# Kernel optimization log

Measured on AMD Instinct MI355X. Metric: run time of the kernel, lower is better.

## Reference

```python
import jax, jax.numpy as jnp
import numpy as np

LEAKAGE = 0.9
RADIUS = 0.1
AVG_DEGREE = 6


def setup_inputs() -> dict:
    key = jax.random.key(0)
    k1, k2, k3, k4, k5 = jax.random.split(key, 5)
    B, T, I, N, O = 16, 2048, 32, 2048, 32
    input_sequence = jax.random.normal(k1, (B, T, I), dtype=jnp.float32)
    # sparse reservoir matrix, uniform(-1,1) with density avg_degree/N, scaled to spectral radius
    A = jax.random.uniform(k2, (N, N), minval=-1.0, maxval=1.0, dtype=jnp.float32)
    mask = jax.random.uniform(k3, (N, N)) < (AVG_DEGREE / N)
    A = jnp.where(mask, A, 0.0)
    # approximate spectral normalization (power-iteration-free surrogate scale)
    A = A * (RADIUS / jnp.max(jnp.abs(jnp.linalg.eigvals(A))).astype(jnp.float32))
    Win = (RADIUS) * (2.0 * jax.random.uniform(k4, (N, I), dtype=jnp.float32) - 1.0)
    Wout_w = jax.random.normal(k5, (O, N), dtype=jnp.float32) / np.sqrt(N)
    return {"input_sequence": input_sequence, "Win": Win, "A": A, "Wout_w": Wout_w, "washout_len": 64}


def reference(input_sequence, Win, A, Wout_w, washout_len):
    # input projection for all timesteps at once (noise_std = 0.0)
    inp = jnp.einsum('bti,ni->btn', input_sequence, Win)  # [B, T, N]
    B = input_sequence.shape[0]
    N = A.shape[0]
    h0 = jnp.zeros((B, N), dtype=input_sequence.dtype)
    At = A.T

    def step(h, u_t):
        # h: [B, N], u_t: [B, N]
        h_new = (1.0 - LEAKAGE) * h + LEAKAGE * jnp.tanh(h @ At + u_t)
        return h_new, h_new

    _, hs = jax.lax.scan(step, h0, jnp.swapaxes(inp, 0, 1))  # hs: [T, B, N]
    hs = jnp.swapaxes(hs, 0, 1)  # [B, T, N]
    h_list = hs[:, washout_len - 1:]  # keep steps i >= washout_len - 1
    return jnp.einsum('btn,on->bto', h_list, Wout_w)
```

## Files before the change

kernel.cpp:

```cpp
#include <hip/hip_runtime.h>
#include <stdint.h>

#define BB 16
#define TT 2048
#define NI 32
#define NN 2048
#define NO 32
#define WASH 64
#define TO (TT - WASH + 1)
#define W 24
#define CH 16
#define UST 18
#define HBST 2056

typedef short bfvec __attribute__((ext_vector_type(8)));
typedef float f4_t  __attribute__((ext_vector_type(4)));

__device__ inline unsigned short f2bf(float f) {
  unsigned int u = __builtin_bit_cast(unsigned int, f);
  unsigned int r = u + 0x7fffu + ((u >> 16) & 1u);
  return (unsigned short)(r >> 16);
}
__device__ inline float bf2f(unsigned short s) {
  unsigned int u = ((unsigned int)s) << 16;
  return __builtin_bit_cast(float, u);
}
__device__ inline float tanh_fast(float x) {
  x = fminf(15.f, fmaxf(-15.f, x));
  float e = __expf(x + x);
  return (e - 1.0f) / (e + 1.0f);
}

__global__ void build_ell(const float* __restrict__ A, uint32_t* __restrict__ ell,
                          uint32_t* __restrict__ deg) {
  int gw = (int)((blockIdx.x * blockDim.x + threadIdx.x) >> 6);
  int lane = (int)(threadIdx.x & 63);
  if (gw >= NN) return;
  const float* row = A + (size_t)gw * NN;
  int base = 0;
  for (int c = 0; c < NN; c += 64) {
    float v = row[c + lane];
    bool nz = (v != 0.0f);
    unsigned long long mask = __ballot(nz);
    int pre = __popcll(mask & ((1ull << lane) - 1ull));
    if (nz) {
      int idx = base + pre;
      if (idx < W) {
        uint32_t packed = (((uint32_t)f2bf(v)) << 16) | (uint32_t)((c + lane) * 4);
        ell[(size_t)gw * W + idx] = packed;
      }
    }
    base += __popcll(mask);
  }
  int d = base < W ? base : W;
  if (lane == 0) deg[gw] = (uint32_t)d;
  for (int k = d + lane; k < W; k += 64) ell[(size_t)gw * W + k] = 0u;
}

__global__ void sortperm(const uint32_t* __restrict__ deg, uint32_t* __restrict__ perm) {
  __shared__ unsigned int hist[32];
  __shared__ unsigned int off[32];
  int tid = (int)threadIdx.x;
  if (tid < 32) hist[tid] = 0;
  __syncthreads();
  for (int r = tid; r < NN; r += 1024) {
    unsigned int d = deg[r]; if (d > 31u) d = 31u;
    atomicAdd(&hist[d], 1u);
  }
  __syncthreads();
  if (tid == 0) {
    unsigned int s = 0;
    for (int i = 0; i < 32; ++i) { off[i] = s; s += hist[i]; }
  }
  __syncthreads();
  for (int r = tid; r < NN; r += 1024) {
    unsigned int d = deg[r]; if (d > 31u) d = 31u;
    unsigned int p = atomicAdd(&off[d], 1u);
    perm[p] = (uint32_t)r;
  }
}

__global__ void build_frags(const float* __restrict__ Win, const float* __restrict__ Wout,
                            uint32_t* __restrict__ winf, uint32_t* __restrict__ woutf) {
  int f = (int)(blockIdx.x * blockDim.x + threadIdx.x);
  if (f < 32768) {
    int reg = f & 3, lane = (f >> 2) & 63, ntg = f >> 8;
    int n = (ntg << 4) + (lane & 15);
    int k = ((lane >> 4) << 3) + reg * 2;
    uint32_t lo = f2bf(Win[(size_t)n * NI + k]);
    uint32_t hi = f2bf(Win[(size_t)n * NI + k + 1]);
    winf[f] = lo | (hi << 16);
  } else {
    int g = f - 32768;
    int reg = g & 3, lane = (g >> 2) & 63, kt = (g >> 8) & 63, ot = g >> 14;
    int o = (ot << 4) + (lane & 15);
    int n = (kt << 5) + ((lane >> 4) << 3) + reg * 2;
    uint32_t lo = f2bf(Wout[(size_t)o * NN + n]);
    uint32_t hi = f2bf(Wout[(size_t)o * NN + n + 1]);
    woutf[g] = lo | (hi << 16);
  }
}

__global__ __launch_bounds__(1024, 1) void rec_kernel(
    const float* __restrict__ x, const uint32_t* __restrict__ ell,
    const uint32_t* __restrict__ deg, const uint32_t* __restrict__ perm,
    const uint32_t* __restrict__ winf, const uint32_t* __restrict__ woutf,
    float* __restrict__ out) {
  extern __shared__ char smem[];
  float* h_a = (float*)smem;
  float* h_b = (float*)(smem + 8192);
  unsigned short* u_lds = (unsigned short*)(smem + 16384);
  float* oscratch = (float*)(smem + 16384);
  unsigned short* hb = (unsigned short*)(smem + 16384 + 73728);

  const int tid = (int)threadIdx.x;
  const int b = (int)blockIdx.x;
  const int lane = tid & 63;
  const int wv = tid >> 6;

  const int r0 = (int)perm[tid];
  const int r1 = (int)perm[2047 - tid];
  int d0 = (int)deg[r0], d1 = (int)deg[r1];
  int m0 = d0, m1 = d1;
  #pragma unroll
  for (int off = 32; off; off >>= 1) {
    m0 = max(m0, __shfl_xor(m0, off));
    m1 = max(m1, __shfl_xor(m1, off));
  }
  m0 = __builtin_amdgcn_readfirstlane(m0);
  m1 = __builtin_amdgcn_readfirstlane(m1);

  uint32_t e0[W], e1[W];
  {
    const uint4* p0 = (const uint4*)(ell + (size_t)r0 * W);
    const uint4* p1 = (const uint4*)(ell + (size_t)r1 * W);
    #pragma unroll
    for (int q = 0; q < W / 4; ++q) {
      uint4 a = p0[q]; uint4 c = p1[q];
      e0[q*4+0]=a.x; e0[q*4+1]=a.y; e0[q*4+2]=a.z; e0[q*4+3]=a.w;
      e1[q*4+0]=c.x; e1[q*4+1]=c.y; e1[q*4+2]=c.z; e1[q*4+3]=c.w;
    }
  }

  h_a[tid] = 0.0f; h_a[tid + 1024] = 0.0f;
  float h0 = 0.0f, h1 = 0.0f;

  const int la15 = lane & 15;
  const int lg = lane >> 4;

  auto step = [&](int tt, const float* hcur, float* hnxt) {
    float y0 = bf2f(u_lds[(size_t)r0 * UST + tt]);
    float y1 = bf2f(u_lds[(size_t)r1 * UST + tt]);
    #pragma unroll
    for (int k = 0; k < W; ++k) {
      if (k >= m0) break;
      uint32_t e = e0[k];
      float v = __builtin_bit_cast(float, e & 0xffff0000u);
      float hv = *(const float*)((const char*)hcur + (e & 0xffffu));
      y0 = __builtin_fmaf(v, hv, y0);
    }
    #pragma unroll
    for (int k = 0; k < W; ++k) {
      if (k >= m1) break;
      uint32_t e = e1[k];
      float v = __builtin_bit_cast(float, e & 0xffff0000u);
      float hv = *(const float*)((const char*)hcur + (e & 0xffffu));
      y1 = __builtin_fmaf(v, hv, y1);
    }
    float hn0 = 0.1f * h0 + 0.9f * tanh_fast(y0);
    float hn1 = 0.1f * h1 + 0.9f * tanh_fast(y1);
    hnxt[r0] = hn0; hnxt[r1] = hn1;
    hb[(size_t)tt * HBST + r0] = f2bf(hn0);
    hb[(size_t)tt * HBST + r1] = f2bf(hn1);
    h0 = hn0; h1 = hn1;
    __syncthreads();
  };

  for (int c = 0; c < TT / CH; ++c) {
    const int t0 = c * CH;

    {
      const float* xp = x + ((size_t)b * TT + (t0 + la15)) * NI + (lg << 3);
      float4 x0 = *(const float4*)xp;
      float4 x1 = *(const float4*)(xp + 4);
      union { unsigned short u16[8]; bfvec v; } af;
      af.u16[0]=f2bf(x0.x); af.u16[1]=f2bf(x0.y); af.u16[2]=f2bf(x0.z); af.u16[3]=f2bf(x0.w);
      af.u16[4]=f2bf(x1.x); af.u16[5]=f2bf(x1.y); af.u16[6]=f2bf(x1.z); af.u16[7]=f2bf(x1.w);
      #pragma unroll
      for (int nt = 0; nt < 8; ++nt) {
        int ntg = (wv << 3) + nt;
        union { uint4 q; bfvec v; } bw;
        bw.q = *(const uint4*)(winf + (((size_t)ntg * 64 + lane) << 2));
        f4_t acc = {0.f, 0.f, 0.f, 0.f};
        acc = __builtin_amdgcn_mfma_f32_16x16x32_bf16(af.v, bw.v, acc, 0, 0, 0);
        int n = (ntg << 4) + la15;
        int tl = lg << 2;
        uint32_t lo = (uint32_t)f2bf(acc[0]) | ((uint32_t)f2bf(acc[1]) << 16);
        uint32_t hi = (uint32_t)f2bf(acc[2]) | ((uint32_t)f2bf(acc[3]) << 16);
        uint32_t* up = (uint32_t*)(u_lds + (size_t)n * UST + tl);
        up[0] = lo; up[1] = hi;
      }
    }
    __syncthreads();

    #pragma unroll 1
    for (int tt = 0; tt < CH; tt += 2) {
      step(tt, h_a, h_b);
      step(tt + 1, h_b, h_a);
    }

    {
      f4_t oa0 = {0.f,0.f,0.f,0.f}, oa1 = {0.f,0.f,0.f,0.f};
      #pragma unroll
      for (int k4 = 0; k4 < 4; ++k4) {
        int kt = (wv << 2) + k4;
        union { uint4 q; bfvec v; } ha, w0, w1;
        ha.q = *(const uint4*)(hb + (size_t)la15 * HBST + (kt << 5) + (lg << 3));
        w0.q = *(const uint4*)(woutf + (((size_t)(kt) * 64 + lane) << 2));
        w1.q = *(const uint4*)(woutf + (((size_t)(64 + kt) * 64 + lane) << 2));
        oa0 = __builtin_amdgcn_mfma_f32_16x16x32_bf16(ha.v, w0.v, oa0, 0, 0, 0);
        oa1 = __builtin_amdgcn_mfma_f32_16x16x32_bf16(ha.v, w1.v, oa1, 0, 0, 0);
      }
      float* os = oscratch + (wv << 9);
      int tb = lg << 2;
      #pragma unroll
      for (int r = 0; r < 4; ++r) os[(tb + r) * 32 + la15] = oa0[r];
      #pragma unroll
      for (int r = 0; r < 4; ++r) os[(tb + r) * 32 + 16 + la15] = oa1[r];
    }
    __syncthreads();
    if (tid < 512) {
      float s = 0.0f;
      #pragma unroll
      for (int w2 = 0; w2 < 16; ++w2) s += oscratch[(w2 << 9) + tid];
      int tg = t0 + (tid >> 5);
      if (tg >= WASH - 1)
        out[((size_t)b * TO + (tg - (WASH - 1))) * NO + (tid & 31)] = s;
    }
    __syncthreads();
  }
}

extern "C" void kernel_launch(void* const* d_in, const int* in_sizes, int n_in,
                              void* d_out, int out_size, void* d_ws, size_t ws_size,
                              hipStream_t stream) {
  (void)in_sizes; (void)n_in; (void)out_size; (void)ws_size;
  const float* x    = (const float*)d_in[0];
  const float* Win  = (const float*)d_in[1];
  const float* A    = (const float*)d_in[2];
  const float* Wout = (const float*)d_in[3];
  float* out = (float*)d_out;

  char* ws = (char*)d_ws;
  uint32_t* ell   = (uint32_t*)(ws);
  uint32_t* deg   = (uint32_t*)(ws + 196608);
  uint32_t* perm  = (uint32_t*)(ws + 204800);
  uint32_t* winf  = (uint32_t*)(ws + 212992);
  uint32_t* woutf = (uint32_t*)(ws + 344064);

  hipFuncSetAttribute((const void*)rec_kernel,
                      hipFuncAttributeMaxDynamicSharedMemorySize, 160 * 1024);

  hipLaunchKernelGGL(build_ell, dim3(512), dim3(256), 0, stream, A, ell, deg);
  hipLaunchKernelGGL(sortperm, dim3(1), dim3(1024), 0, stream, deg, perm);
  hipLaunchKernelGGL(build_frags, dim3(256), dim3(256), 0, stream, Win, Wout, winf, woutf);
  hipLaunchKernelGGL(rec_kernel, dim3(16), dim3(1024), 155904, stream,
                     x, ell, deg, perm, winf, woutf, out);
}
```

Baseline: 3.063 ms.

## Renumber reservoir rows by degree and schedule ELL gathers to avoid LDS bank conflicts

```diff
diff --git a/kernel.cpp b/kernel.cpp
--- a/kernel.cpp
+++ b/kernel.cpp
@@ -57,53 +57,107 @@
   for (int k = d + lane; k < W; k += 64) ell[(size_t)gw * W + k] = 0u;
 }
 
-__global__ void sortperm(const uint32_t* __restrict__ deg, uint32_t* __restrict__ perm) {
-  __shared__ unsigned int hist[32];
-  __shared__ unsigned int off[32];
+__global__ void sortperm(const uint32_t* __restrict__ deg, uint32_t* __restrict__ perm,
+                         uint32_t* __restrict__ invp) {
+  __shared__ int dg[NN];
   int tid = (int)threadIdx.x;
-  if (tid < 32) hist[tid] = 0;
+  dg[tid] = (int)deg[tid];
+  dg[tid + 1024] = (int)deg[tid + 1024];
   __syncthreads();
   for (int r = tid; r < NN; r += 1024) {
-    unsigned int d = deg[r]; if (d > 31u) d = 31u;
-    atomicAdd(&hist[d], 1u);
+    int d = dg[r];
+    int rank = 0;
+    for (int j = 0; j < NN; ++j) {
+      int dj = dg[j];
+      rank += (dj < d) || (dj == d && j < r);
+    }
+    perm[rank] = (uint32_t)r;
+    invp[r] = (uint32_t)rank;
+  }
+}
+
+__global__ void schedule_ell(const uint32_t* __restrict__ ell_in, const uint32_t* __restrict__ deg,
+                             const uint32_t* __restrict__ perm, const uint32_t* __restrict__ invp,
+                             uint32_t* __restrict__ ell_out, uint32_t* __restrict__ slen) {
+  __shared__ uint32_t ent[64][W];
+  __shared__ uint32_t outp[64][W];
+  __shared__ int nent[64];
+  __shared__ uint32_t used[64];
+  __shared__ int Ssh;
+  int blk = (int)blockIdx.x;
+  int t = (int)threadIdx.x;
+  int rs = blk * 64 + t;
+  int ro = (int)perm[rs];
+  int d = (int)deg[ro]; if (d > W) d = W;
+  nent[t] = d; used[t] = 0u;
+  for (int k = 0; k < d; ++k) {
+    uint32_t e = ell_in[(size_t)ro * W + k];
+    uint32_t col = (e & 0xffffu) >> 2;
+    uint32_t cs = invp[col];
+    ent[t][k] = (e & 0xffff0000u) | (cs << 2);
   }
   __syncthreads();
-  if (tid == 0) {
-    unsigned int s = 0;
-    for (int i = 0; i < 32; ++i) { off[i] = s; s += hist[i]; }
+  if (t == 0) {
+    int S = 0;
+    for (int i = 0; i < 64; ++i) S = max(S, nent[i]);
+    for (int s = 0; s < S; ++s) {
+      unsigned char bank_cnt[32];
+      for (int b = 0; b < 32; ++b) bank_cnt[b] = 0;
+      for (int i = 0; i < 64; ++i) {
+        int r = (i + s * 19) & 63;
+        if (s < nent[r]) {
+          int sel = -1, selb = 0, best = 256;
+          for (int k = 0; k < nent[r]; ++k) {
+            if ((used[r] >> k) & 1u) continue;
+            int b = (int)((ent[r][k] >> 2) & 31u);
+            if ((int)bank_cnt[b] < best) { best = bank_cnt[b]; sel = k; selb = b; }
+          }
+          used[r] |= (1u << sel);
+          bank_cnt[selb]++;
+          outp[r][s] = ent[r][sel];
+        } else {
+          int bk = 0;
+          for (int b = 1; b < 32; ++b) if (bank_cnt[b] < bank_cnt[bk]) bk = b;
+          bank_cnt[bk]++;
+          outp[r][s] = ((uint32_t)bk << 2);
+        }
+      }
+    }
+    Ssh = S;
+    slen[blk] = (uint32_t)S;
   }
   __syncthreads();
-  for (int r = tid; r < NN; r += 1024) {
-    unsigned int d = deg[r]; if (d > 31u) d = 31u;
-    unsigned int p = atomicAdd(&off[d], 1u);
-    perm[p] = (uint32_t)r;
-  }
+  int S = Ssh;
+  for (int k = 0; k < W; ++k)
+    ell_out[(size_t)rs * W + k] = (k < S) ? outp[t][k] : 0u;
 }
 
 __global__ void build_frags(const float* __restrict__ Win, const float* __restrict__ Wout,
+                            const uint32_t* __restrict__ perm,
                             uint32_t* __restrict__ winf, uint32_t* __restrict__ woutf) {
   int f = (int)(blockIdx.x * blockDim.x + threadIdx.x);
   if (f < 32768) {
     int reg = f & 3, lane = (f >> 2) & 63, ntg = f >> 8;
     int n = (ntg << 4) + (lane & 15);
     int k = ((lane >> 4) << 3) + reg * 2;
-    uint32_t lo = f2bf(Win[(size_t)n * NI + k]);
-    uint32_t hi = f2bf(Win[(size_t)n * NI + k + 1]);
+    int np = (int)perm[n];
+    uint32_t lo = f2bf(Win[(size_t)np * NI + k]);
+    uint32_t hi = f2bf(Win[(size_t)np * NI + k + 1]);
     winf[f] = lo | (hi << 16);
   } else {
     int g = f - 32768;
     int reg = g & 3, lane = (g >> 2) & 63, kt = (g >> 8) & 63, ot = g >> 14;
     int o = (ot << 4) + (lane & 15);
     int n = (kt << 5) + ((lane >> 4) << 3) + reg * 2;
-    uint32_t lo = f2bf(Wout[(size_t)o * NN + n]);
-    uint32_t hi = f2bf(Wout[(size_t)o * NN + n + 1]);
+    uint32_t lo = f2bf(Wout[(size_t)o * NN + (int)perm[n]]);
+    uint32_t hi = f2bf(Wout[(size_t)o * NN + (int)perm[n + 1]]);
     woutf[g] = lo | (hi << 16);
   }
 }
 
 __global__ __launch_bounds__(1024, 1) void rec_kernel(
     const float* __restrict__ x, const uint32_t* __restrict__ ell,
-    const uint32_t* __restrict__ deg, const uint32_t* __restrict__ perm,
+    const uint32_t* __restrict__ slen,
     const uint32_t* __restrict__ winf, const uint32_t* __restrict__ woutf,
     float* __restrict__ out) {
   extern __shared__ char smem[];
@@ -118,17 +172,10 @@
   const int lane = tid & 63;
   const int wv = tid >> 6;
 
-  const int r0 = (int)perm[tid];
-  const int r1 = (int)perm[2047 - tid];
-  int d0 = (int)deg[r0], d1 = (int)deg[r1];
-  int m0 = d0, m1 = d1;
-  #pragma unroll
-  for (int off = 32; off; off >>= 1) {
-    m0 = max(m0, __shfl_xor(m0, off));
-    m1 = max(m1, __shfl_xor(m1, off));
-  }
-  m0 = __builtin_amdgcn_readfirstlane(m0);
-  m1 = __builtin_amdgcn_readfirstlane(m1);
+  const int r0 = tid;
+  const int r1 = 2047 - tid;
+  int m0 = __builtin_amdgcn_readfirstlane((int)slen[wv]);
+  int m1 = __builtin_amdgcn_readfirstlane((int)slen[31 - wv]);
 
   uint32_t e0[W], e1[W];
   {
@@ -255,15 +302,19 @@
   uint32_t* ell   = (uint32_t*)(ws);
   uint32_t* deg   = (uint32_t*)(ws + 196608);
   uint32_t* perm  = (uint32_t*)(ws + 204800);
-  uint32_t* winf  = (uint32_t*)(ws + 212992);
-  uint32_t* woutf = (uint32_t*)(ws + 344064);
+  uint32_t* invp  = (uint32_t*)(ws + 212992);
+  uint32_t* slen  = (uint32_t*)(ws + 221184);
+  uint32_t* ell2  = (uint32_t*)(ws + 221312);
+  uint32_t* winf  = (uint32_t*)(ws + 417920);
+  uint32_t* woutf = (uint32_t*)(ws + 548992);
 
   hipFuncSetAttribute((const void*)rec_kernel,
                       hipFuncAttributeMaxDynamicSharedMemorySize, 160 * 1024);
 
   hipLaunchKernelGGL(build_ell, dim3(512), dim3(256), 0, stream, A, ell, deg);
-  hipLaunchKernelGGL(sortperm, dim3(1), dim3(1024), 0, stream, deg, perm);
-  hipLaunchKernelGGL(build_frags, dim3(256), dim3(256), 0, stream, Win, Wout, winf, woutf);
+  hipLaunchKernelGGL(sortperm, dim3(1), dim3(1024), 0, stream, deg, perm, invp);
+  hipLaunchKernelGGL(schedule_ell, dim3(32), dim3(64), 0, stream, ell, deg, perm, invp, ell2, slen);
+  hipLaunchKernelGGL(build_frags, dim3(256), dim3(256), 0, stream, Win, Wout, perm, winf, woutf);
   hipLaunchKernelGGL(rec_kernel, dim3(16), dim3(1024), 155904, stream,
-                     x, ell, deg, perm, winf, woutf, out);
-}
+                     x, ell2, slen, winf, woutf, out);
+}
```

Measured after the change: 6.104 ms. 99.3% more time.
